# Kernel tuning notes

Hardware: AMD Instinct MI355X
Metric: run time of the kernel (lower is better)

## Reference

```python
import jax, jax.numpy as jnp
import numpy as np
import math

B, S, D_MODEL, H = 2, 2048, 2048, 16
HD = D_MODEL // H  # head_dim = 128


def setup_inputs() -> dict:
    key = jax.random.key(0)
    ks = jax.random.split(key, 10)
    x = jax.random.normal(ks[0], (B, S, D_MODEL), dtype=jnp.float32)
    # RoPE tables: interleaved-pair layout matching rotate_half (adjacent dims form pairs)
    inv_freq = 1.0 / (10000.0 ** (jnp.arange(0, HD, 2, dtype=jnp.float32) / HD))  # [HD/2]
    angles = jnp.arange(S, dtype=jnp.float32)[:, None] * inv_freq[None, :]        # [S, HD/2]
    angles = jnp.repeat(angles, 2, axis=-1)                                       # [S, HD]
    cos, sin = jnp.cos(angles), jnp.sin(angles)
    # causal mask (1 = keep), broadcastable to [B,H,S,S]
    attn_mask = jnp.tril(jnp.ones((S, S), dtype=bool))[None, None]
    scale = 1.0 / math.sqrt(D_MODEL)
    Wq = jax.random.normal(ks[1], (D_MODEL, D_MODEL), dtype=jnp.float32) * scale
    Wk = jax.random.normal(ks[2], (D_MODEL, D_MODEL), dtype=jnp.float32) * scale
    Wv = jax.random.normal(ks[3], (D_MODEL, D_MODEL), dtype=jnp.float32) * scale
    Wo = jax.random.normal(ks[4], (D_MODEL, D_MODEL), dtype=jnp.float32) * scale
    bq = jnp.zeros((D_MODEL,), jnp.float32)
    bk = jnp.zeros((D_MODEL,), jnp.float32)
    bv = jnp.zeros((D_MODEL,), jnp.float32)
    bo = jnp.zeros((D_MODEL,), jnp.float32)
    return {"x": x, "cos": cos, "sin": sin, "attn_mask": attn_mask,
            "Wq": Wq, "bq": bq, "Wk": Wk, "bk": bk, "Wv": Wv, "bv": bv, "Wo": Wo, "bo": bo}


def _rotate_half(x):
    # pairs adjacent dims: (x0,x1) -> (-x1,x0)
    xr = x.reshape(*x.shape[:-1], -1, 2)
    x1, x2 = xr[..., 0], xr[..., 1]
    return jnp.stack([-x2, x1], axis=-1).reshape(x.shape)


def reference(x, cos, sin, attn_mask, Wq, bq, Wk, bk, Wv, bv, Wo, bo):
    b, s, _ = x.shape
    q = (x @ Wq.T + bq).reshape(b, s, H, HD).transpose(0, 2, 1, 3)  # [B,H,S,HD]
    k = (x @ Wk.T + bk).reshape(b, s, H, HD).transpose(0, 2, 1, 3)
    v = (x @ Wv.T + bv).reshape(b, s, H, HD).transpose(0, 2, 1, 3)
    c = cos[None, None]  # [1,1,S,HD]
    sn = sin[None, None]
    q = q * c + _rotate_half(q) * sn
    k = k * c + _rotate_half(k) * sn
    scores = jnp.einsum('bhqd,bhkd->bhqk', q, k) / math.sqrt(HD)  # [B,H,S,S]
    scores = jnp.where(attn_mask, scores, -jnp.inf)
    attn = jax.nn.softmax(scores, axis=-1)
    out = jnp.einsum('bhqk,bhkd->bhqd', attn, v)  # [B,H,S,HD]
    out = out.transpose(0, 2, 1, 3).reshape(b, s, H * HD)
    return out @ Wo.T + bo
```

## Files before the change

### kernel.cpp

```cpp
#include <hip/hip_runtime.h>
#include <math.h>

typedef __attribute__((ext_vector_type(8))) __bf16 bf16x8;
typedef __attribute__((ext_vector_type(4))) float f32x4;
typedef __attribute__((ext_vector_type(4))) unsigned short us4;
typedef unsigned short u16;
typedef unsigned int u32;

#define DEVI static __device__ __forceinline__

DEVI u16 f2bf(float f) {
  union { float f; unsigned u; } v; v.f = f;
  unsigned r = v.u + 0x7fffu + ((v.u >> 16) & 1u);
  return (u16)(r >> 16);
}

DEVI void async16(const void* g, void* l) {
  __builtin_amdgcn_global_load_lds((const __attribute__((address_space(1))) void*)g,
                                   (__attribute__((address_space(3))) void*)l, 16, 0, 0);
}

DEVI u32 pkbf(float lo, float hi) {
  u32 r;
  asm("v_cvt_pk_bf16_f32 %0, %1, %2" : "=v"(r) : "v"(lo), "v"(hi));
  return r;
}

__global__ __launch_bounds__(256) void cast_bf16(const float* __restrict__ in,
                                                 u16* __restrict__ out, int n) {
  int i = (blockIdx.x * 256 + threadIdx.x) * 4;
  if (i >= n) return;
  float4 v = *(const float4*)(in + i);
  us4 o = { f2bf(v.x), f2bf(v.y), f2bf(v.z), f2bf(v.w) };
  *(us4*)(out + i) = o;
}

__global__ __launch_bounds__(512, 2)
void gemm8p(const u16* __restrict__ A,
            const u16* __restrict__ W0, const u16* __restrict__ W1, const u16* __restrict__ W2,
            const float* __restrict__ biasQ, const float* __restrict__ biasK,
            const float* __restrict__ biasV,
            const float* __restrict__ cosT, const float* __restrict__ sinT,
            void* __restrict__ out0, void* __restrict__ out1, void* __restrict__ out2,
            int ntn, int qkv)
{
  __shared__ __align__(16) char lds[3 * 49152];
  const int t = threadIdx.x, w = t >> 6, lane = t & 63;
  const int lrow = lane & 15, g = lane >> 4, lk8 = g * 8;
  const int xcd = blockIdx.x & 7, bi = blockIdx.x >> 3;
  const int ntpx = ntn >> 3;
  const int nt = xcd * ntpx + (bi % ntpx);
  const int mt = bi / ntpx;
  const int slab = qkv ? (nt >> 4) : 3;
  const u16* Bp = (slab == 1) ? W1 : (slab == 2) ? W2 : W0;
  const int brow = mt * 256;
  const int bcol = (qkv ? (nt & 15) : nt) * 128;
  const int wm = w >> 1, wn = w & 1;

  size_t soff[6];
#pragma unroll
  for (int j = 0; j < 6; ++j) {
    int p = j * 8192 + t * 16;
    int pr = (j < 4) ? p : (p - 32768);
    int r = pr >> 7;
    int c = ((pr ^ ((r & 7) << 4)) & 127) >> 1;
    soff[j] = (j < 4) ? ((size_t)(brow + r) * 2048 + c)
                      : ((size_t)(bcol + r) * 2048 + c);
  }
  auto stage = [&](int tile, int j, char* buf) {
    const u16* src = (j < 4) ? A : Bp;
    async16(src + soff[j] + tile * 64, buf + j * 8192 + t * 16);
  };

  int offA[4][2], offB[4][2];
#pragma unroll
  for (int m = 0; m < 4; ++m)
#pragma unroll
    for (int kk = 0; kk < 2; ++kk) {
      const int c = (lk8 + kk * 32) * 2;
      const int ra = wm * 64 + m * 16 + lrow;
      offA[m][kk] = (ra * 128 + c) ^ ((ra & 7) << 4);
      const int rb = wn * 64 + m * 16 + lrow;
      offB[m][kk] = 32768 + ((rb * 128 + c) ^ ((rb & 7) << 4));
    }

  f32x4 acc[4][4] = {};

#pragma unroll
  for (int j = 0; j < 6; ++j) stage(0, j, lds);
#pragma unroll
  for (int j = 0; j < 6; ++j) stage(1, j, lds + 49152);
  asm volatile("s_waitcnt vmcnt(6)" ::: "memory");
  __builtin_amdgcn_s_barrier();

  for (int tt = 0; tt < 32; ++tt) {
    char* cur = lds + (tt % 3) * 49152;
    char* nxt = lds + ((tt + 2) % 3) * 49152;
    const bool st = (tt + 2) < 32;

    bf16x8 bfr[4][2], afr[2][2];
#pragma unroll
    for (int n = 0; n < 4; ++n)
#pragma unroll
      for (int kk = 0; kk < 2; ++kk) bfr[n][kk] = *(const bf16x8*)(cur + offB[n][kk]);
#pragma unroll
    for (int m = 0; m < 2; ++m)
#pragma unroll
      for (int kk = 0; kk < 2; ++kk) afr[m][kk] = *(const bf16x8*)(cur + offA[m][kk]);
    if (st) { stage(tt + 2, 0, nxt); stage(tt + 2, 1, nxt); stage(tt + 2, 2, nxt); }
    __builtin_amdgcn_s_barrier();
    asm volatile("s_waitcnt lgkmcnt(0)" ::: "memory");
    __builtin_amdgcn_sched_barrier(0);
    __builtin_amdgcn_s_setprio(1);
#pragma unroll
    for (int m = 0; m < 2; ++m)
#pragma unroll
      for (int n = 0; n < 4; ++n)
#pragma unroll
        for (int kk = 0; kk < 2; ++kk)
          acc[m][n] = __builtin_amdgcn_mfma_f32_16x16x32_bf16(afr[m][kk], bfr[n][kk], acc[m][n], 0, 0, 0);
    __builtin_amdgcn_s_setprio(0);
    __builtin_amdgcn_s_barrier();

#pragma unroll
    for (int m = 0; m < 2; ++m)
#pragma unroll
      for (int kk = 0; kk < 2; ++kk) afr[m][kk] = *(const bf16x8*)(cur + offA[m + 2][kk]);
    if (st) { stage(tt + 2, 3, nxt); stage(tt + 2, 4, nxt); stage(tt + 2, 5, nxt); }
    if (tt < 31) {
      if (st) asm volatile("s_waitcnt vmcnt(6)" ::: "memory");
      else    asm volatile("s_waitcnt vmcnt(0)" ::: "memory");
    }
    __builtin_amdgcn_s_barrier();
    asm volatile("s_waitcnt lgkmcnt(0)" ::: "memory");
    __builtin_amdgcn_sched_barrier(0);
    __builtin_amdgcn_s_setprio(1);
#pragma unroll
    for (int m = 0; m < 2; ++m)
#pragma unroll
      for (int n = 0; n < 4; ++n)
#pragma unroll
        for (int kk = 0; kk < 2; ++kk)
          acc[m + 2][n] = __builtin_amdgcn_mfma_f32_16x16x32_bf16(afr[m][kk], bfr[n][kk], acc[m + 2][n], 0, 0, 0);
    __builtin_amdgcn_s_setprio(0);
    __builtin_amdgcn_s_barrier();
  }

  const int g4 = g * 4;
#pragma unroll
  for (int mi = 0; mi < 4; ++mi) {
#pragma unroll
    for (int ni = 0; ni < 4; ++ni) {
      f32x4 v = acc[mi][ni];
      const int row0 = brow + wm * 64 + mi * 16 + g4;
      const int cols = bcol + wn * 64 + ni * 16 + lrow;
      if (slab == 3) {
        float* O = (float*)out0;
        const float bv = biasQ[cols];
#pragma unroll
        for (int r = 0; r < 4; ++r)
          O[(size_t)(row0 + r) * 2048 + cols] = v[r] + bv;
      } else if (slab == 2) {
        u16* O = (u16*)out2;
        const float bv = biasV[cols];
        const int h = cols >> 7, d = cols & 127;
        const int bb = row0 >> 11, s = row0 & 2047;
        us4 ov;
#pragma unroll
        for (int r = 0; r < 4; ++r) ov[r] = f2bf(v[r] + bv);
        const int l = s & 63;
        const int kt = l >> 4, g2 = (l >> 2) & 3;
        const int c = ((kt >> 1) << 5) + (g2 << 3) + ((kt & 1) << 2);
        u16* base = O + ((size_t)(bb * 16 + h) * 128 + d) * 2048 + (s & ~63);
        *(us4*)((char*)base + ((unsigned)(c << 1) ^ (unsigned)((d & 7) << 4))) = ov;
      } else {
        u16* O = (u16*)(slab ? out1 : out0);
        const float bv = slab ? biasK[cols] : biasQ[cols];
        const int h = cols >> 7, d = cols & 127;
        const float sgn = (d & 1) ? 1.f : -1.f;
        const float QSCL = 0.08838834764831845f * 1.44269504088896340f;
#pragma unroll
        for (int r = 0; r < 4; ++r) {
          const int row = row0 + r, bb = row >> 11, s = row & 2047;
          float q = v[r] + bv;
          float p = __shfl_xor(q, 1);
          float o = q * cosT[s * 128 + d] + sgn * p * sinT[s * 128 + d];
          u16* base = O + ((size_t)(bb * 16 + h) * 2048 + s) * 128;
          if (slab == 0) {
            base[d] = f2bf(o * QSCL);
          } else {
            *(u16*)((char*)base + (((unsigned)(d << 1)) ^ (unsigned)((s & 7) << 4))) = f2bf(o);
          }
        }
      }
    }
  }
}

__global__ __launch_bounds__(256, 2)
void attn_fwd(const u16* __restrict__ Q, const u16* __restrict__ K,
              const u16* __restrict__ Vt, u16* __restrict__ AO)
{
  __shared__ __align__(16) u16 Ks[2][64 * 128];
  __shared__ __align__(16) u16 Vs[2][128 * 64];
  const int t = threadIdx.x, w = t >> 6, lane = t & 63;
  const int lrow = lane & 15, g = lane >> 4, lk8 = g * 8;
  const int id = blockIdx.x;
  const int bh = (id & 7) | (((id >> 3) & 3) << 3);
  const int pr = id >> 5;
  const u16* Qg = Q + (size_t)bh * 2048 * 128;
  const u16* Kg = K + (size_t)bh * 2048 * 128;
  const u16* Vg = Vt + (size_t)bh * 128 * 2048;
  const int bb = bh >> 4, h = bh & 15;

  for (int half = 0; half < 2; ++half) {
    const int qt = half ? (31 - pr) : pr;
    const int q0 = qt * 64, qw = q0 + w * 16;
    const int nkv = qt + 1;
    const int qg = qw + lrow;

    bf16x8 qf[4];
#pragma unroll
    for (int c = 0; c < 4; ++c)
      qf[c] = *(const bf16x8*)(Qg + (size_t)(qw + lrow) * 128 + lk8 + c * 32);

    f32x4 acc_o[8] = {};
    float m = -1e30f, lsum = 0.f;

    auto stage = [&](int i, int b) {
#pragma unroll
      for (int r = 0; r < 4; ++r) {
        int e = (r * 256 + t) * 8;
        async16(Kg + (size_t)i * 8192 + e, &Ks[b][r * 2048 + w * 512]);
        async16(Vg + (size_t)(e >> 6) * 2048 + i * 64 + (e & 63), &Vs[b][r * 2048 + w * 512]);
      }
    };

    stage(0, 0);
    for (int i = 0; i < nkv; ++i) {
      const int cur = i & 1;
      const bool pfch = (i + 1) < nkv;
      if (pfch) stage(i + 1, cur ^ 1);
      if (pfch) asm volatile("s_waitcnt vmcnt(8)" ::: "memory");
      else      asm volatile("s_waitcnt vmcnt(0)" ::: "memory");
      __builtin_amdgcn_s_barrier();
      __builtin_amdgcn_sched_barrier(0);

      f32x4 sc[4];
      __builtin_amdgcn_s_setprio(1);
#pragma unroll
      for (int kt = 0; kt < 4; ++kt) {
        f32x4 s = {};
        const int krow = kt * 16 + lrow;
        const char* kbase = (const char*)(&Ks[cur][krow * 128]);
        const unsigned sw = (unsigned)((krow & 7) << 4);
#pragma unroll
        for (int c = 0; c < 4; ++c) {
          bf16x8 kf = *(const bf16x8*)(kbase + ((unsigned)((lk8 + c * 32) << 1) ^ sw));
          s = __builtin_amdgcn_mfma_f32_16x16x32_bf16(kf, qf[c], s, 0, 0, 0);
        }
        sc[kt] = s;
      }
      __builtin_amdgcn_s_setprio(0);

      float p[4][4];
      const bool lastblk = (i == qt);
      if (lastblk) {
#pragma unroll
        for (int kt = 0; kt < 4; ++kt)
#pragma unroll
          for (int r = 0; r < 4; ++r) {
            int kg = i * 64 + kt * 16 + g * 4 + r;
            p[kt][r] = (kg > qg) ? -1e30f : sc[kt][r];
          }
      } else {
#pragma unroll
        for (int kt = 0; kt < 4; ++kt)
#pragma unroll
          for (int r = 0; r < 4; ++r) p[kt][r] = sc[kt][r];
      }

      float mm = p[0][0];
#pragma unroll
      for (int kt = 0; kt < 4; ++kt)
#pragma unroll
        for (int r = 0; r < 4; ++r) mm = fmaxf(mm, p[kt][r]);
      mm = fmaxf(mm, __shfl_xor(mm, 16));
      mm = fmaxf(mm, __shfl_xor(mm, 32));

      float rs = 0.f;
      if (__any(mm > m + 8.f)) {
        const float mn = fmaxf(m, mm);
        const float corr = exp2f(m - mn);
        m = mn;
#pragma unroll
        for (int kt = 0; kt < 4; ++kt)
#pragma unroll
          for (int r = 0; r < 4; ++r) { p[kt][r] = exp2f(p[kt][r] - m); rs += p[kt][r]; }
        rs += __shfl_xor(rs, 16);
        rs += __shfl_xor(rs, 32);
        lsum = lsum * corr + rs;
#pragma unroll
        for (int nt = 0; nt < 8; ++nt)
#pragma unroll
          for (int r = 0; r < 4; ++r) acc_o[nt][r] *= corr;
      } else {
#pragma unroll
        for (int kt = 0; kt < 4; ++kt)
#pragma unroll
          for (int r = 0; r < 4; ++r) { p[kt][r] = exp2f(p[kt][r] - m); rs += p[kt][r]; }
        rs += __shfl_xor(rs, 16);
        rs += __shfl_xor(rs, 32);
        lsum += rs;
      }

      bf16x8 pb[2];
#pragma unroll
      for (int kc = 0; kc < 2; ++kc) {
        union { u32 d[4]; bf16x8 v; } u;
        u.d[0] = pkbf(p[2 * kc][0], p[2 * kc][1]);
        u.d[1] = pkbf(p[2 * kc][2], p[2 * kc][3]);
        u.d[2] = pkbf(p[2 * kc + 1][0], p[2 * kc + 1][1]);
        u.d[3] = pkbf(p[2 * kc + 1][2], p[2 * kc + 1][3]);
        pb[kc] = u.v;
      }

      __builtin_amdgcn_s_setprio(1);
#pragma unroll
      for (int nt = 0; nt < 8; ++nt) {
        const int vrow = nt * 16 + lrow;
        const char* vbase = (const char*)(&Vs[cur][vrow * 64]);
        const unsigned sw2 = (unsigned)((vrow & 7) << 4);
#pragma unroll
        for (int kc = 0; kc < 2; ++kc) {
          bf16x8 vf = *(const bf16x8*)(vbase + ((unsigned)((lk8 + kc * 32) << 1) ^ sw2));
          acc_o[nt] = __builtin_amdgcn_mfma_f32_16x16x32_bf16(vf, pb[kc], acc_o[nt], 0, 0, 0);
        }
      }
      __builtin_amdgcn_s_setprio(0);
      __builtin_amdgcn_s_barrier();
    }

    const float inv_l = 1.f / lsum;
#pragma unroll
    for (int nt = 0; nt < 8; ++nt) {
      us4 ov;
#pragma unroll
      for (int r = 0; r < 4; ++r) ov[r] = f2bf(acc_o[nt][r] * inv_l);
      *(us4*)(AO + ((size_t)(bb * 2048 + qg)) * 2048 + h * 128 + nt * 16 + g * 4) = ov;
    }
  }
}

extern "C" void kernel_launch(void* const* d_in, const int* in_sizes, int n_in,
                              void* d_out, int out_size, void* d_ws, size_t ws_size,
                              hipStream_t stream) {
  const float* x    = (const float*)d_in[0];
  const float* cosT = (const float*)d_in[1];
  const float* sinT = (const float*)d_in[2];
  const float* Wq   = (const float*)d_in[4];
  const float* bq   = (const float*)d_in[5];
  const float* Wk   = (const float*)d_in[6];
  const float* bk   = (const float*)d_in[7];
  const float* Wv   = (const float*)d_in[8];
  const float* bv   = (const float*)d_in[9];
  const float* Wo   = (const float*)d_in[10];
  const float* bo   = (const float*)d_in[11];
  float* out = (float*)d_out;

  char* ws = (char*)d_ws;
  u16* xb  = (u16*)(ws);
  u16* Wqb = (u16*)(ws + (16u << 20));
  u16* Wkb = (u16*)(ws + (24u << 20));
  u16* Wvb = (u16*)(ws + (32u << 20));
  u16* Wob = (u16*)(ws + (40u << 20));
  u16* Qb  = (u16*)(ws + (48u << 20));
  u16* Kb  = (u16*)(ws + (64u << 20));
  u16* Vtb = (u16*)(ws + (80u << 20));
  u16* AOb = (u16*)(ws + (96u << 20));

  cast_bf16<<<8192, 256, 0, stream>>>(x,  xb,  4096 * 2048);
  cast_bf16<<<4096, 256, 0, stream>>>(Wq, Wqb, 2048 * 2048);
  cast_bf16<<<4096, 256, 0, stream>>>(Wk, Wkb, 2048 * 2048);
  cast_bf16<<<4096, 256, 0, stream>>>(Wv, Wvb, 2048 * 2048);
  cast_bf16<<<4096, 256, 0, stream>>>(Wo, Wob, 2048 * 2048);

  gemm8p<<<768, 512, 0, stream>>>(xb, Wqb, Wkb, Wvb, bq, bk, bv, cosT, sinT,
                                  (void*)Qb, (void*)Kb, (void*)Vtb, 48, 1);

  attn_fwd<<<512, 256, 0, stream>>>(Qb, Kb, Vtb, AOb);

  gemm8p<<<256, 512, 0, stream>>>(AOb, Wob, Wob, Wob, bo, bo, bo, nullptr, nullptr,
                                  (void*)out, nullptr, nullptr, 16, 0);
}
```

Baseline: 274.2 us.

## Switch projection GEMMs to 256x256 tiles with double-buffered LDS pipeline

```diff
diff --git a/kernel.cpp b/kernel.cpp
--- a/kernel.cpp
+++ b/kernel.cpp
@@ -36,123 +36,139 @@
 }
 
 __global__ __launch_bounds__(512, 2)
-void gemm8p(const u16* __restrict__ A,
-            const u16* __restrict__ W0, const u16* __restrict__ W1, const u16* __restrict__ W2,
-            const float* __restrict__ biasQ, const float* __restrict__ biasK,
-            const float* __restrict__ biasV,
-            const float* __restrict__ cosT, const float* __restrict__ sinT,
-            void* __restrict__ out0, void* __restrict__ out1, void* __restrict__ out2,
-            int ntn, int qkv)
+void gemm256(const u16* __restrict__ A,
+             const u16* __restrict__ W0, const u16* __restrict__ W1, const u16* __restrict__ W2,
+             const float* __restrict__ biasQ, const float* __restrict__ biasK,
+             const float* __restrict__ biasV,
+             const float* __restrict__ cosT, const float* __restrict__ sinT,
+             void* __restrict__ out0, void* __restrict__ out1, void* __restrict__ out2,
+             int ntn, int qkv)
 {
-  __shared__ __align__(16) char lds[3 * 49152];
+  __shared__ __align__(16) char lds[2 * 65536];
   const int t = threadIdx.x, w = t >> 6, lane = t & 63;
   const int lrow = lane & 15, g = lane >> 4, lk8 = g * 8;
   const int xcd = blockIdx.x & 7, bi = blockIdx.x >> 3;
   const int ntpx = ntn >> 3;
-  const int nt = xcd * ntpx + (bi % ntpx);
-  const int mt = bi / ntpx;
-  const int slab = qkv ? (nt >> 4) : 3;
+  const int nt = xcd * ntpx + (ntpx > 1 ? bi % ntpx : 0);
+  const int mt = ntpx > 1 ? bi / ntpx : bi;
+  const int slab = qkv ? (nt >> 3) : 3;
   const u16* Bp = (slab == 1) ? W1 : (slab == 2) ? W2 : W0;
   const int brow = mt * 256;
-  const int bcol = (qkv ? (nt & 15) : nt) * 128;
-  const int wm = w >> 1, wn = w & 1;
-
-  size_t soff[6];
-#pragma unroll
-  for (int j = 0; j < 6; ++j) {
-    int p = j * 8192 + t * 16;
-    int pr = (j < 4) ? p : (p - 32768);
-    int r = pr >> 7;
-    int c = ((pr ^ ((r & 7) << 4)) & 127) >> 1;
-    soff[j] = (j < 4) ? ((size_t)(brow + r) * 2048 + c)
-                      : ((size_t)(bcol + r) * 2048 + c);
+  const int bcol = (qkv ? (nt & 7) : nt) * 256;
+  const int wm = w >> 2, wn = w & 3;
+
+  u32 soff[8];
+#pragma unroll
+  for (int j = 0; j < 8; ++j) {
+    const int q = (j & 3) * 8192 + t * 16;
+    const int row = q >> 7;
+    const int cb = (q ^ ((row & 7) << 4)) & 127;
+    soff[j] = (u32)(((j < 4 ? brow : bcol) + row) * 2048 + (cb >> 1));
   }
   auto stage = [&](int tile, int j, char* buf) {
     const u16* src = (j < 4) ? A : Bp;
     async16(src + soff[j] + tile * 64, buf + j * 8192 + t * 16);
   };
 
-  int offA[4][2], offB[4][2];
-#pragma unroll
-  for (int m = 0; m < 4; ++m)
+  int offA[8][2], offB[4][2];
+#pragma unroll
+  for (int mi = 0; mi < 8; ++mi)
 #pragma unroll
     for (int kk = 0; kk < 2; ++kk) {
-      const int c = (lk8 + kk * 32) * 2;
-      const int ra = wm * 64 + m * 16 + lrow;
-      offA[m][kk] = (ra * 128 + c) ^ ((ra & 7) << 4);
-      const int rb = wn * 64 + m * 16 + lrow;
-      offB[m][kk] = 32768 + ((rb * 128 + c) ^ ((rb & 7) << 4));
+      const int row = wm * 128 + mi * 16 + lrow;
+      offA[mi][kk] = (row * 128 + (kk * 32 + lk8) * 2) ^ ((row & 7) << 4);
     }
-
-  f32x4 acc[4][4] = {};
-
-#pragma unroll
-  for (int j = 0; j < 6; ++j) stage(0, j, lds);
-#pragma unroll
-  for (int j = 0; j < 6; ++j) stage(1, j, lds + 49152);
-  asm volatile("s_waitcnt vmcnt(6)" ::: "memory");
-  __builtin_amdgcn_s_barrier();
+#pragma unroll
+  for (int ni = 0; ni < 4; ++ni)
+#pragma unroll
+    for (int kk = 0; kk < 2; ++kk) {
+      const int row = wn * 64 + ni * 16 + lrow;
+      offB[ni][kk] = 32768 + ((row * 128 + (kk * 32 + lk8) * 2) ^ ((row & 7) << 4));
+    }
+
+  f32x4 acc[8][4] = {};
+  bf16x8 alo[4][2], ahi[4][2], bfr[4][2];
+
+  stage(0, 0, lds); stage(0, 2, lds); stage(0, 4, lds); stage(0, 5, lds);
+  stage(0, 6, lds); stage(0, 7, lds); stage(0, 1, lds); stage(0, 3, lds);
 
   for (int tt = 0; tt < 32; ++tt) {
-    char* cur = lds + (tt % 3) * 49152;
-    char* nxt = lds + ((tt + 2) % 3) * 49152;
-    const bool st = (tt + 2) < 32;
-
-    bf16x8 bfr[4][2], afr[2][2];
-#pragma unroll
-    for (int n = 0; n < 4; ++n)
-#pragma unroll
-      for (int kk = 0; kk < 2; ++kk) bfr[n][kk] = *(const bf16x8*)(cur + offB[n][kk]);
-#pragma unroll
-    for (int m = 0; m < 2; ++m)
-#pragma unroll
-      for (int kk = 0; kk < 2; ++kk) afr[m][kk] = *(const bf16x8*)(cur + offA[m][kk]);
-    if (st) { stage(tt + 2, 0, nxt); stage(tt + 2, 1, nxt); stage(tt + 2, 2, nxt); }
-    __builtin_amdgcn_s_barrier();
+    char* cur = lds + (tt & 1) * 65536;
+    char* nxt = lds + ((tt + 1) & 1) * 65536;
+    const bool st = tt < 31;
+
+    if (st) { stage(tt + 1, 0, nxt); stage(tt + 1, 2, nxt); }
+    if (st) asm volatile("s_waitcnt vmcnt(4)" ::: "memory");
+    else    asm volatile("s_waitcnt vmcnt(2)" ::: "memory");
+    __builtin_amdgcn_s_barrier();
+#pragma unroll
+    for (int mi = 0; mi < 4; ++mi)
+#pragma unroll
+      for (int kk = 0; kk < 2; ++kk) alo[mi][kk] = *(const bf16x8*)(cur + offA[mi][kk]);
+#pragma unroll
+    for (int ni = 0; ni < 4; ++ni) bfr[ni][0] = *(const bf16x8*)(cur + offB[ni][0]);
     asm volatile("s_waitcnt lgkmcnt(0)" ::: "memory");
     __builtin_amdgcn_sched_barrier(0);
     __builtin_amdgcn_s_setprio(1);
 #pragma unroll
-    for (int m = 0; m < 2; ++m)
-#pragma unroll
-      for (int n = 0; n < 4; ++n)
-#pragma unroll
-        for (int kk = 0; kk < 2; ++kk)
-          acc[m][n] = __builtin_amdgcn_mfma_f32_16x16x32_bf16(afr[m][kk], bfr[n][kk], acc[m][n], 0, 0, 0);
+    for (int mi = 0; mi < 4; ++mi)
+#pragma unroll
+      for (int ni = 0; ni < 4; ++ni)
+        acc[mi][ni] = __builtin_amdgcn_mfma_f32_16x16x32_bf16(alo[mi][0], bfr[ni][0], acc[mi][ni], 0, 0, 0);
     __builtin_amdgcn_s_setprio(0);
     __builtin_amdgcn_s_barrier();
 
-#pragma unroll
-    for (int m = 0; m < 2; ++m)
-#pragma unroll
-      for (int kk = 0; kk < 2; ++kk) afr[m][kk] = *(const bf16x8*)(cur + offA[m + 2][kk]);
-    if (st) { stage(tt + 2, 3, nxt); stage(tt + 2, 4, nxt); stage(tt + 2, 5, nxt); }
-    if (tt < 31) {
-      if (st) asm volatile("s_waitcnt vmcnt(6)" ::: "memory");
-      else    asm volatile("s_waitcnt vmcnt(0)" ::: "memory");
-    }
-    __builtin_amdgcn_s_barrier();
+    if (st) { stage(tt + 1, 4, nxt); stage(tt + 1, 5, nxt); }
+    if (st) asm volatile("s_waitcnt vmcnt(4)" ::: "memory");
+    else    asm volatile("s_waitcnt vmcnt(0)" ::: "memory");
+    __builtin_amdgcn_s_barrier();
+#pragma unroll
+    for (int ni = 0; ni < 4; ++ni) bfr[ni][1] = *(const bf16x8*)(cur + offB[ni][1]);
+#pragma unroll
+    for (int mi = 0; mi < 4; ++mi) ahi[mi][0] = *(const bf16x8*)(cur + offA[mi + 4][0]);
     asm volatile("s_waitcnt lgkmcnt(0)" ::: "memory");
     __builtin_amdgcn_sched_barrier(0);
     __builtin_amdgcn_s_setprio(1);
 #pragma unroll
-    for (int m = 0; m < 2; ++m)
-#pragma unroll
-      for (int n = 0; n < 4; ++n)
-#pragma unroll
-        for (int kk = 0; kk < 2; ++kk)
-          acc[m + 2][n] = __builtin_amdgcn_mfma_f32_16x16x32_bf16(afr[m][kk], bfr[n][kk], acc[m + 2][n], 0, 0, 0);
+    for (int mi = 0; mi < 4; ++mi)
+#pragma unroll
+      for (int ni = 0; ni < 4; ++ni)
+        acc[mi][ni] = __builtin_amdgcn_mfma_f32_16x16x32_bf16(alo[mi][1], bfr[ni][1], acc[mi][ni], 0, 0, 0);
     __builtin_amdgcn_s_setprio(0);
     __builtin_amdgcn_s_barrier();
+
+    if (st) { stage(tt + 1, 6, nxt); stage(tt + 1, 7, nxt); }
+#pragma unroll
+    for (int mi = 0; mi < 4; ++mi) ahi[mi][1] = *(const bf16x8*)(cur + offA[mi + 4][1]);
+    __builtin_amdgcn_s_setprio(1);
+#pragma unroll
+    for (int mi = 0; mi < 4; ++mi)
+#pragma unroll
+      for (int ni = 0; ni < 4; ++ni)
+        acc[mi + 4][ni] = __builtin_amdgcn_mfma_f32_16x16x32_bf16(ahi[mi][0], bfr[ni][0], acc[mi + 4][ni], 0, 0, 0);
+    __builtin_amdgcn_s_setprio(0);
+    __builtin_amdgcn_s_barrier();
+
+    if (st) { stage(tt + 1, 1, nxt); stage(tt + 1, 3, nxt); }
+    asm volatile("s_waitcnt lgkmcnt(0)" ::: "memory");
+    __builtin_amdgcn_sched_barrier(0);
+    __builtin_amdgcn_s_setprio(1);
+#pragma unroll
+    for (int mi = 0; mi < 4; ++mi)
+#pragma unroll
+      for (int ni = 0; ni < 4; ++ni)
+        acc[mi + 4][ni] = __builtin_amdgcn_mfma_f32_16x16x32_bf16(ahi[mi][1], bfr[ni][1], acc[mi + 4][ni], 0, 0, 0);
+    __builtin_amdgcn_s_setprio(0);
+    __builtin_amdgcn_s_barrier();
   }
 
   const int g4 = g * 4;
 #pragma unroll
-  for (int mi = 0; mi < 4; ++mi) {
+  for (int mi = 0; mi < 8; ++mi) {
 #pragma unroll
     for (int ni = 0; ni < 4; ++ni) {
       f32x4 v = acc[mi][ni];
-      const int row0 = brow + wm * 64 + mi * 16 + g4;
+      const int row0 = brow + wm * 128 + mi * 16 + g4;
       const int cols = bcol + wn * 64 + ni * 16 + lrow;
       if (slab == 3) {
         float* O = (float*)out0;
@@ -385,11 +401,11 @@
   cast_bf16<<<4096, 256, 0, stream>>>(Wv, Wvb, 2048 * 2048);
   cast_bf16<<<4096, 256, 0, stream>>>(Wo, Wob, 2048 * 2048);
 
-  gemm8p<<<768, 512, 0, stream>>>(xb, Wqb, Wkb, Wvb, bq, bk, bv, cosT, sinT,
-                                  (void*)Qb, (void*)Kb, (void*)Vtb, 48, 1);
+  gemm256<<<384, 512, 0, stream>>>(xb, Wqb, Wkb, Wvb, bq, bk, bv, cosT, sinT,
+                                   (void*)Qb, (void*)Kb, (void*)Vtb, 24, 1);
 
   attn_fwd<<<512, 256, 0, stream>>>(Qb, Kb, Vtb, AOb);
 
-  gemm8p<<<256, 512, 0, stream>>>(AOb, Wob, Wob, Wob, bo, bo, bo, nullptr, nullptr,
-                                  (void*)out, nullptr, nullptr, 16, 0);
-}
+  gemm256<<<128, 512, 0, stream>>>(AOb, Wob, Wob, Wob, bo, bo, bo, nullptr, nullptr,
+                                   (void*)out, nullptr, nullptr, 8, 0);
+}
```

Result: slower. 314.0 us (+14.5%).
